# Optimization experiments

Hardware: AMD Instinct MI355X
Metric: run time of the kernel (lower is better)

The kernel has to match this reference:

```python
import jax, jax.numpy as jnp
import numpy as np

N_NODES = 100000
N_EDGES = 1600000
F_IN = 64
H = 64


def gcn_conv(x, W, b, src, dst, ew):
    """PyG GCNConv with edge weights, symmetric norm, self-loops (weight 1)."""
    n = x.shape[0]
    xw = x @ W                                        # [N, H] linear transform first
    deg = jnp.zeros((n,), x.dtype).at[dst].add(ew) + 1.0  # +1 for self-loop weight
    dinv = jax.lax.rsqrt(deg)                         # deg >= 1, safe
    norm = dinv[src] * ew * dinv[dst]                 # [E]
    agg = jnp.zeros_like(xw).at[dst].add(norm[:, None] * xw[src])  # gather-scale-scatter
    agg = agg + (dinv * dinv)[:, None] * xw           # self-loop term: deg^-1 * xw
    return agg + b


def setup_inputs() -> dict:
    key = jax.random.key(0)
    ks = jax.random.split(key, 10)
    x = jax.random.normal(ks[0], (N_NODES, F_IN), jnp.float32)
    edge_index = jax.random.randint(ks[1], (2, N_EDGES), 0, N_NODES, dtype=jnp.int64)
    # distances in km in [0, 500): exp(-(d/200)^2) gives meaningful weight spread
    edge_attr = jax.random.uniform(ks[2], (N_EDGES,), jnp.float32) * 500.0
    s = 1.0 / np.sqrt(H)
    W1 = jax.random.normal(ks[3], (F_IN, H), jnp.float32) * s
    b1 = jnp.zeros((H,), jnp.float32)
    W2 = jax.random.normal(ks[4], (H, H), jnp.float32) * s
    b2 = jnp.zeros((H,), jnp.float32)
    W3 = jax.random.normal(ks[5], (H, 1), jnp.float32) * s
    b3 = jnp.zeros((1,), jnp.float32)
    return {"x": x, "edge_index": edge_index, "edge_attr": edge_attr,
            "W1": W1, "b1": b1, "W2": W2, "b2": b2, "W3": W3, "b3": b3}


def reference(x, edge_index, edge_attr, W1, b1, W2, b2, W3, b3):
    src, dst = edge_index[0], edge_index[1]
    ew = jnp.exp(-jnp.square(edge_attr / 200.0))      # Gaussian distance kernel
    h = jax.nn.relu(gcn_conv(x, W1, b1, src, dst, ew))
    # dropout p=0.1 is identity at eval time (reference runs in eval mode)
    h = jax.nn.relu(gcn_conv(h, W2, b2, src, dst, ew))
    h = gcn_conv(h, W3, b3, src, dst, ew)
    return h[:, 0]                                    # squeeze(-1) -> [N]
```

## Files before the change

kernel.cpp:

```cpp
#include <hip/hip_runtime.h>
#include <cstdint>

#define N_NODES 100000
#define N_EDGES 1600000
#define NBUCKET 196
#define NPB_SHIFT 9
#define NPB 512
#define P1_CHUNK 4096
#define NB_P1 391
#define NBG 1563
#define BSW_CAP 9216
#define CSR_CAP 12800

typedef int iv4 __attribute__((ext_vector_type(4)));
typedef unsigned short usv8 __attribute__((ext_vector_type(8)));

__device__ __forceinline__ unsigned short f2bf(float x) {
    unsigned u = __float_as_uint(x);
    unsigned r = ((u >> 16) & 1u) + 0x7FFFu;
    return (unsigned short)((u + r) >> 16);
}
__device__ __forceinline__ float bf2f(unsigned short v) {
    return __uint_as_float((unsigned)v << 16);
}


__global__ __launch_bounds__(256) void k_init(int* __restrict__ gcursor) {
    int i = threadIdx.x;
    if (i < NBUCKET) gcursor[i] = i * BSW_CAP;
}

struct P1Shared {
    uint2 stage[P1_CHUNK];
    unsigned char stage_bkt[P1_CHUNK];
    int cnt[256];
    int lbase[256];
    int gbase[256];
};
struct GemmShared { float sX[64][65]; float sW[64][65]; };

__global__ __launch_bounds__(256) void k_p1gemm(const int* __restrict__ dst,
                                                const int* __restrict__ srcarr,
                                                const float* __restrict__ ea,
                                                int* gcursor,
                                                uint2* __restrict__ bsw,
                                                const float* __restrict__ X,
                                                const float* __restrict__ W,
                                                float* __restrict__ Y) {
    __shared__ union { P1Shared p; GemmShared g; } sm;
    int t = threadIdx.x;
    if (blockIdx.x < NB_P1) {
        sm.p.cnt[t] = 0;
        __syncthreads();
        int e0 = blockIdx.x * P1_CHUNK;
        unsigned int dr[16];
#pragma unroll
        for (int i = 0; i < 4; ++i) {
            int idx = e0 + (t + i * 256) * 4;
            if (idx + 3 < N_EDGES) {
                int4 d4 = *reinterpret_cast<const int4*>(&dst[idx]);
                int r0 = atomicAdd(&sm.p.cnt[d4.x >> NPB_SHIFT], 1);
                int r1 = atomicAdd(&sm.p.cnt[d4.y >> NPB_SHIFT], 1);
                int r2 = atomicAdd(&sm.p.cnt[d4.z >> NPB_SHIFT], 1);
                int r3 = atomicAdd(&sm.p.cnt[d4.w >> NPB_SHIFT], 1);
                dr[i * 4 + 0] = ((unsigned)d4.x << 12) | (unsigned)r0;
                dr[i * 4 + 1] = ((unsigned)d4.y << 12) | (unsigned)r1;
                dr[i * 4 + 2] = ((unsigned)d4.z << 12) | (unsigned)r2;
                dr[i * 4 + 3] = ((unsigned)d4.w << 12) | (unsigned)r3;
            } else {
#pragma unroll
                for (int k = 0; k < 4; ++k) dr[i * 4 + k] = 0xFFFFFFFFu;
            }
        }
        __syncthreads();
        int v = sm.p.cnt[t];
        sm.p.lbase[t] = v;
        __syncthreads();
        for (int off = 1; off < 256; off <<= 1) {
            int u = (t >= off) ? sm.p.lbase[t - off] : 0;
            __syncthreads();
            sm.p.lbase[t] += u;
            __syncthreads();
        }
        int ex = sm.p.lbase[t] - v;
        if (t < NBUCKET) sm.p.gbase[t] = atomicAdd(&gcursor[t], v);
        __syncthreads();
        sm.p.lbase[t] = ex;
        __syncthreads();
#pragma unroll
        for (int i = 0; i < 4; ++i) {
            int idx = e0 + (t + i * 256) * 4;
            if (idx + 3 < N_EDGES) {
                int4 s4 = *reinterpret_cast<const int4*>(&srcarr[idx]);
                float4 a4 = *reinterpret_cast<const float4*>(&ea[idx]);
                float t0 = a4.x * (1.0f / 200.0f), t1 = a4.y * (1.0f / 200.0f);
                float t2 = a4.z * (1.0f / 200.0f), t3 = a4.w * (1.0f / 200.0f);
                int   ss[4] = {s4.x, s4.y, s4.z, s4.w};
                float ww[4] = {__expf(-t0 * t0), __expf(-t1 * t1),
                               __expf(-t2 * t2), __expf(-t3 * t3)};
#pragma unroll
                for (int k = 0; k < 4; ++k) {
                    unsigned drv = dr[i * 4 + k];
                    int d = drv >> 12, r = drv & 0xFFF;
                    int b = d >> NPB_SHIFT, dloc = d & (NPB - 1);
                    int pos = sm.p.lbase[b] + r;
                    sm.p.stage[pos] = make_uint2(((unsigned)dloc << 17) | (unsigned)ss[k],
                                                 __float_as_uint(ww[k]));
                    sm.p.stage_bkt[pos] = (unsigned char)b;
                }
            }
        }
        __syncthreads();
        int n_valid = min(P1_CHUNK, N_EDGES - e0);
        for (int j = t; j < n_valid; j += 256) {
            int b = sm.p.stage_bkt[j];
            int pos = sm.p.gbase[b] + (j - sm.p.lbase[b]);
            bsw[pos] = sm.p.stage[j];
        }
        return;
    }
    int rb = (blockIdx.x - NB_P1) * 64;
#pragma unroll
    for (int i = 0; i < 16; ++i) {
        int idx = t + i * 256;
        int r = idx >> 6, c = idx & 63;
        sm.g.sW[r][c] = W[idx];
        int gr = rb + r;
        sm.g.sX[r][c] = (gr < N_NODES) ? X[(size_t)gr * 64 + c] : 0.0f;
    }
    __syncthreads();
    int tr = (t >> 4) * 4;
    int tc = (t & 15) * 4;
    float acc[4][4] = {{0.f}};
#pragma unroll 8
    for (int k = 0; k < 64; ++k) {
        float xv[4], wv[4];
#pragma unroll
        for (int i = 0; i < 4; ++i) xv[i] = sm.g.sX[tr + i][k];
#pragma unroll
        for (int j = 0; j < 4; ++j) wv[j] = sm.g.sW[k][tc + j];
#pragma unroll
        for (int i = 0; i < 4; ++i)
#pragma unroll
            for (int j = 0; j < 4; ++j) acc[i][j] = fmaf(xv[i], wv[j], acc[i][j]);
    }
#pragma unroll
    for (int i = 0; i < 4; ++i) {
        int gr = rb + tr + i;
        if (gr < N_NODES) {
            float4 v = make_float4(acc[i][0], acc[i][1], acc[i][2], acc[i][3]);
            *reinterpret_cast<float4*>(&Y[(size_t)gr * 64 + tc]) = v;
        }
    }
}

__global__ __launch_bounds__(1024) void k_p2(const uint2* __restrict__ bsw,
                                             const int* __restrict__ gcursor,
                                             int2* __restrict__ rowinfo,
                                             int2* __restrict__ csr,
                                             float* __restrict__ dinv) {
    __shared__ int cnt[NPB];
    __shared__ int prp[NPB];
    __shared__ int cur[NPB];
    __shared__ float degw[NPB];
    int t = threadIdx.x;
    int b = blockIdx.x;
    if (t < NPB) { cnt[t] = 0; degw[t] = 0.0f; }
    __syncthreads();
    int segb = b * BSW_CAP;
    int sege = gcursor[b];
    int pbase = b * CSR_CAP;
    for (int j = segb + t; j < sege; j += 1024)
        atomicAdd(&cnt[bsw[j].x >> 17], 1);
    __syncthreads();
    int raw = (t < NPB) ? cnt[t] : 0;
    int pad = (raw + 7) & ~7;
    if (t < NPB) prp[t] = pad;
    __syncthreads();
    for (int off = 1; off < NPB; off <<= 1) {
        int u = (t >= off && t < NPB) ? prp[t - off] : 0;
        __syncthreads();
        if (t < NPB) prp[t] += u;
        __syncthreads();
    }
    if (t < NPB) { prp[t] -= pad; cur[t] = prp[t]; }
    __syncthreads();
    int node = (b << NPB_SHIFT) + t;
    if (t < NPB && node < N_NODES)
        rowinfo[node] = make_int2(pbase + prp[t], pad >> 3);
    for (int j = segb + t; j < sege; j += 1024) {
        uint2 v = bsw[j];
        int dloc = (int)(v.x >> 17);
        int src  = (int)(v.x & 0x1FFFFu);
        int pos = atomicAdd(&cur[dloc], 1);
        csr[pbase + pos] = make_int2(src, (int)v.y);
        atomicAdd(&degw[dloc], __uint_as_float(v.y));
    }
    __syncthreads();
    if (t < NPB && node < N_NODES) {
        dinv[node] = rsqrtf(1.0f + degw[t]);
        int begin = pbase + prp[t];
        for (int j = raw; j < pad; ++j) csr[begin + j] = make_int2(node, 0);
    }
}

__global__ __launch_bounds__(256) void k_scale(const float* __restrict__ XW,
                                               const float* __restrict__ dinv,
                                               unsigned short* __restrict__ XWs) {
    int g = blockIdx.x * 256 + threadIdx.x;
    int base = g * 8;
    if (base >= N_NODES * 64) return;
    float d = dinv[base >> 6];
    float4 v0 = *reinterpret_cast<const float4*>(XW + base);
    float4 v1 = *reinterpret_cast<const float4*>(XW + base + 4);
    usv8 r;
    r.s0 = f2bf(d * v0.x); r.s1 = f2bf(d * v0.y);
    r.s2 = f2bf(d * v0.z); r.s3 = f2bf(d * v0.w);
    r.s4 = f2bf(d * v1.x); r.s5 = f2bf(d * v1.y);
    r.s6 = f2bf(d * v1.z); r.s7 = f2bf(d * v1.w);
    *reinterpret_cast<usv8*>(XWs + base) = r;
}


__global__ __launch_bounds__(256) void k_gemm64s(const float* __restrict__ X,
                                                 const float* __restrict__ W,
                                                 const float* __restrict__ dinv,
                                                 unsigned short* __restrict__ XWs) {
    __shared__ float sX[64][65];
    __shared__ float sW[64][65];
    int t = threadIdx.x;
    int rb = blockIdx.x * 64;
#pragma unroll
    for (int i = 0; i < 16; ++i) {
        int idx = t + i * 256;
        int r = idx >> 6, c = idx & 63;
        sW[r][c] = W[idx];
        int gr = rb + r;
        sX[r][c] = (gr < N_NODES) ? X[(size_t)gr * 64 + c] : 0.0f;
    }
    __syncthreads();
    int tr = (t >> 4) * 4;
    int tc = (t & 15) * 4;
    float acc[4][4] = {{0.f}};
#pragma unroll 8
    for (int k = 0; k < 64; ++k) {
        float xv[4], wv[4];
#pragma unroll
        for (int i = 0; i < 4; ++i) xv[i] = sX[tr + i][k];
#pragma unroll
        for (int j = 0; j < 4; ++j) wv[j] = sW[k][tc + j];
#pragma unroll
        for (int i = 0; i < 4; ++i)
#pragma unroll
            for (int j = 0; j < 4; ++j) acc[i][j] = fmaf(xv[i], wv[j], acc[i][j]);
    }
#pragma unroll
    for (int i = 0; i < 4; ++i) {
        int gr = rb + tr + i;
        if (gr < N_NODES) {
            float d = dinv[gr];
            ushort4 v;
            v.x = f2bf(d * acc[i][0]); v.y = f2bf(d * acc[i][1]);
            v.z = f2bf(d * acc[i][2]); v.w = f2bf(d * acc[i][3]);
            *reinterpret_cast<ushort4*>(&XWs[((unsigned)gr << 6) + tc]) = v;
        }
    }
}

template <int MODE>
__global__ __launch_bounds__(256) void k_agg64(const unsigned short* __restrict__ XWs,
                                               const int* __restrict__ csr_i,
                                               const int2* __restrict__ rowinfo,
                                               const float* __restrict__ dinv,
                                               const float* __restrict__ bias,
                                               float* __restrict__ OUT,
                                               const float* __restrict__ W3) {
    int wid0 = (blockIdx.x * 256 + threadIdx.x) >> 6;
    if (wid0 >= N_NODES) return;
    int wid = __builtin_amdgcn_readfirstlane(wid0);
    unsigned f = threadIdx.x & 63;
    float di = dinv[wid];
    float selfs = bf2f(XWs[((unsigned)wid << 6) + f]);
    int2 ri = rowinfo[wid];
    int rbase = __builtin_amdgcn_readfirstlane(ri.x);
    int nb    = __builtin_amdgcn_readfirstlane(ri.y);
    const int* pc = csr_i + ((size_t)rbase * 2);
    float a[8] = {0.f, 0.f, 0.f, 0.f, 0.f, 0.f, 0.f, 0.f};
    for (int it = 0; it < nb; ++it, pc += 16) {
        int s0 = pc[0],  w0 = pc[1],  s1 = pc[2],  w1 = pc[3];
        int s2 = pc[4],  w2 = pc[5],  s3 = pc[6],  w3 = pc[7];
        int s4 = pc[8],  w4 = pc[9],  s5 = pc[10], w5 = pc[11];
        int s6 = pc[12], w6 = pc[13], s7 = pc[14], w7 = pc[15];
        float r0 = bf2f(XWs[((unsigned)s0 << 6) + f]);
        float r1 = bf2f(XWs[((unsigned)s1 << 6) + f]);
        float r2 = bf2f(XWs[((unsigned)s2 << 6) + f]);
        float r3 = bf2f(XWs[((unsigned)s3 << 6) + f]);
        float r4 = bf2f(XWs[((unsigned)s4 << 6) + f]);
        float r5 = bf2f(XWs[((unsigned)s5 << 6) + f]);
        float r6 = bf2f(XWs[((unsigned)s6 << 6) + f]);
        float r7 = bf2f(XWs[((unsigned)s7 << 6) + f]);
        a[0] = fmaf(__int_as_float(w0), r0, a[0]);
        a[1] = fmaf(__int_as_float(w1), r1, a[1]);
        a[2] = fmaf(__int_as_float(w2), r2, a[2]);
        a[3] = fmaf(__int_as_float(w3), r3, a[3]);
        a[4] = fmaf(__int_as_float(w4), r4, a[4]);
        a[5] = fmaf(__int_as_float(w5), r5, a[5]);
        a[6] = fmaf(__int_as_float(w6), r6, a[6]);
        a[7] = fmaf(__int_as_float(w7), r7, a[7]);
    }
    float esum = ((a[0] + a[1]) + (a[2] + a[3])) + ((a[4] + a[5]) + (a[6] + a[7]));
    float acc = di * (selfs + esum) + bias[f];
    acc = fmaxf(acc, 0.0f);
    if (MODE == 0) {
        OUT[((unsigned)wid << 6) + f] = acc;
    } else {
        float v = acc * W3[f];
#pragma unroll
        for (int off = 32; off > 0; off >>= 1) v += __shfl_down(v, off, 64);
        if (f == 0) OUT[wid] = di * v;
    }
}

__global__ __launch_bounds__(256) void k_agg_scalar(const float* __restrict__ xw3s,
                                                    const int2* __restrict__ csr,
                                                    const int2* __restrict__ rowinfo,
                                                    const float* __restrict__ dinv,
                                                    const float* __restrict__ b3,
                                                    float* __restrict__ out) {
    int i = blockIdx.x * 256 + threadIdx.x;
    if (i >= N_NODES) return;
    float di = dinv[i];
    int2 ri = rowinfo[i];
    const iv4* p = reinterpret_cast<const iv4*>(csr + ri.x);
    int nb = ri.y;
    float a0 = 0.f, a1 = 0.f, a2 = 0.f, a3 = 0.f;
    for (int it = 0; it < nb; ++it, p += 4) {
        iv4 q0 = __builtin_nontemporal_load(p);
        iv4 q1 = __builtin_nontemporal_load(p + 1);
        iv4 q2 = __builtin_nontemporal_load(p + 2);
        iv4 q3 = __builtin_nontemporal_load(p + 3);
        a0 = fmaf(__int_as_float(q0.y), xw3s[q0.x], a0);
        a1 = fmaf(__int_as_float(q0.w), xw3s[q0.z], a1);
        a2 = fmaf(__int_as_float(q1.y), xw3s[q1.x], a2);
        a3 = fmaf(__int_as_float(q1.w), xw3s[q1.z], a3);
        a0 = fmaf(__int_as_float(q2.y), xw3s[q2.x], a0);
        a1 = fmaf(__int_as_float(q2.w), xw3s[q2.z], a1);
        a2 = fmaf(__int_as_float(q3.y), xw3s[q3.x], a2);
        a3 = fmaf(__int_as_float(q3.w), xw3s[q3.z], a3);
    }
    out[i] = di * (xw3s[i] + (a0 + a1) + (a2 + a3)) + b3[0];
}


extern "C" void kernel_launch(void* const* d_in, const int* in_sizes, int n_in,
                              void* d_out, int out_size, void* d_ws, size_t ws_size,
                              hipStream_t stream) {
    const float* x  = (const float*)d_in[0];
    const int*   ei = (const int*)d_in[1];
    const float* ea = (const float*)d_in[2];
    const float* W1 = (const float*)d_in[3];
    const float* b1 = (const float*)d_in[4];
    const float* W2 = (const float*)d_in[5];
    const float* b2 = (const float*)d_in[6];
    const float* W3 = (const float*)d_in[7];
    const float* b3 = (const float*)d_in[8];
    float* out = (float*)d_out;
    const int* srcarr = ei;
    const int* dstarr = ei + N_EDGES;

    char* ws = (char*)d_ws;
    size_t off = 0;
    auto alloc = [&](size_t bytes) -> void* {
        void* p = ws + off;
        off = (off + bytes + 255) & ~(size_t)255;
        return p;
    };
    float* dinv     = (float*)alloc((size_t)N_NODES * 4);
    int2*  rowinfo  = (int2*) alloc((size_t)N_NODES * 8);
    int*   gcursor  = (int*)  alloc(NBUCKET * 4);
    float* xw3s     = (float*)alloc((size_t)N_NODES * 4);
    void*  region   = alloc((size_t)NBUCKET * BSW_CAP * 8);
    uint2*          bsw  = (uint2*)region;
    unsigned short* XWs1 = (unsigned short*)region;
    int2*  csr      = (int2*) alloc((size_t)NBUCKET * CSR_CAP * 8);
    float* bufA     = (float*)alloc((size_t)N_NODES * 64 * 4);
    float* bufB     = (float*)alloc((size_t)N_NODES * 64 * 4);
    unsigned short* XWs2 = (unsigned short*)bufA;

    const int nbW = N_NODES / 4;
    const int nbN = (N_NODES + 255) / 256;
    const int nbS = (N_NODES * 64 / 8 + 255) / 256;

    k_init<<<1, 256, 0, stream>>>(gcursor);
    k_p1gemm<<<NB_P1 + NBG, 256, 0, stream>>>(dstarr, srcarr, ea, gcursor,
                                              bsw, x, W1, bufA);
    k_p2<<<NBUCKET, 1024, 0, stream>>>(bsw, gcursor, rowinfo, csr, dinv);
    k_scale<<<nbS, 256, 0, stream>>>(bufA, dinv, XWs1);

    k_agg64<0><<<nbW, 256, 0, stream>>>(XWs1, (const int*)csr, rowinfo, dinv, b1, bufB, nullptr);
    k_gemm64s<<<NBG, 256, 0, stream>>>(bufB, W2, dinv, XWs2);
    k_agg64<1><<<nbW, 256, 0, stream>>>(XWs2, (const int*)csr, rowinfo, dinv, b2, xw3s, W3);
    k_agg_scalar<<<nbN, 256, 0, stream>>>(xw3s, csr, rowinfo, dinv, b3, out);
}
```

Measured before the change: 206.8 us.

## Split wavefront into two half-waves over edges, pad CSR to 16, shrink partition chunks

```diff
diff --git a/kernel.cpp b/kernel.cpp
--- a/kernel.cpp
+++ b/kernel.cpp
@@ -6,11 +6,11 @@
 #define NBUCKET 196
 #define NPB_SHIFT 9
 #define NPB 512
-#define P1_CHUNK 4096
-#define NB_P1 391
+#define P1_CHUNK 2048
+#define NB_P1 782
 #define NBG 1563
 #define BSW_CAP 9216
-#define CSR_CAP 12800
+#define CSR_CAP 17408
 
 typedef int iv4 __attribute__((ext_vector_type(4)));
 typedef unsigned short usv8 __attribute__((ext_vector_type(8)));
@@ -37,7 +37,7 @@
     int lbase[256];
     int gbase[256];
 };
-struct GemmShared { float sX[64][65]; float sW[64][65]; };
+struct GemmShared { float sW[64][65]; float sX[32][65]; };
 
 __global__ __launch_bounds__(256) void k_p1gemm(const int* __restrict__ dst,
                                                 const int* __restrict__ srcarr,
@@ -53,9 +53,9 @@
         sm.p.cnt[t] = 0;
         __syncthreads();
         int e0 = blockIdx.x * P1_CHUNK;
-        unsigned int dr[16];
-#pragma unroll
-        for (int i = 0; i < 4; ++i) {
+        unsigned int dr[8];
+#pragma unroll
+        for (int i = 0; i < 2; ++i) {
             int idx = e0 + (t + i * 256) * 4;
             if (idx + 3 < N_EDGES) {
                 int4 d4 = *reinterpret_cast<const int4*>(&dst[idx]);
@@ -88,7 +88,7 @@
         sm.p.lbase[t] = ex;
         __syncthreads();
 #pragma unroll
-        for (int i = 0; i < 4; ++i) {
+        for (int i = 0; i < 2; ++i) {
             int idx = e0 + (t + i * 256) * 4;
             if (idx + 3 < N_EDGES) {
                 int4 s4 = *reinterpret_cast<const int4*>(&srcarr[idx]);
@@ -123,33 +123,41 @@
 #pragma unroll
     for (int i = 0; i < 16; ++i) {
         int idx = t + i * 256;
-        int r = idx >> 6, c = idx & 63;
-        sm.g.sW[r][c] = W[idx];
-        int gr = rb + r;
-        sm.g.sX[r][c] = (gr < N_NODES) ? X[(size_t)gr * 64 + c] : 0.0f;
-    }
-    __syncthreads();
-    int tr = (t >> 4) * 4;
-    int tc = (t & 15) * 4;
-    float acc[4][4] = {{0.f}};
+        sm.g.sW[idx >> 6][idx & 63] = W[idx];
+    }
+    for (int half = 0; half < 2; ++half) {
+        int rb2 = rb + half * 32;
+        __syncthreads();
+#pragma unroll
+        for (int i = 0; i < 8; ++i) {
+            int idx = t + i * 256;
+            int r = idx >> 6, c = idx & 63;
+            int gr = rb2 + r;
+            sm.g.sX[r][c] = (gr < N_NODES) ? X[(size_t)gr * 64 + c] : 0.0f;
+        }
+        __syncthreads();
+        int tr = (t >> 4) * 2;
+        int tc = (t & 15) * 4;
+        float acc[2][4] = {{0.f, 0.f, 0.f, 0.f}, {0.f, 0.f, 0.f, 0.f}};
 #pragma unroll 8
-    for (int k = 0; k < 64; ++k) {
-        float xv[4], wv[4];
-#pragma unroll
-        for (int i = 0; i < 4; ++i) xv[i] = sm.g.sX[tr + i][k];
-#pragma unroll
-        for (int j = 0; j < 4; ++j) wv[j] = sm.g.sW[k][tc + j];
-#pragma unroll
-        for (int i = 0; i < 4; ++i)
-#pragma unroll
-            for (int j = 0; j < 4; ++j) acc[i][j] = fmaf(xv[i], wv[j], acc[i][j]);
-    }
-#pragma unroll
-    for (int i = 0; i < 4; ++i) {
-        int gr = rb + tr + i;
-        if (gr < N_NODES) {
-            float4 v = make_float4(acc[i][0], acc[i][1], acc[i][2], acc[i][3]);
-            *reinterpret_cast<float4*>(&Y[(size_t)gr * 64 + tc]) = v;
+        for (int k = 0; k < 64; ++k) {
+            float xv0 = sm.g.sX[tr][k], xv1 = sm.g.sX[tr + 1][k];
+            float wv[4];
+#pragma unroll
+            for (int j = 0; j < 4; ++j) wv[j] = sm.g.sW[k][tc + j];
+#pragma unroll
+            for (int j = 0; j < 4; ++j) {
+                acc[0][j] = fmaf(xv0, wv[j], acc[0][j]);
+                acc[1][j] = fmaf(xv1, wv[j], acc[1][j]);
+            }
+        }
+#pragma unroll
+        for (int i = 0; i < 2; ++i) {
+            int gr = rb2 + tr + i;
+            if (gr < N_NODES) {
+                float4 v = make_float4(acc[i][0], acc[i][1], acc[i][2], acc[i][3]);
+                *reinterpret_cast<float4*>(&Y[(size_t)gr * 64 + tc]) = v;
+            }
         }
     }
 }
@@ -174,7 +182,7 @@
         atomicAdd(&cnt[bsw[j].x >> 17], 1);
     __syncthreads();
     int raw = (t < NPB) ? cnt[t] : 0;
-    int pad = (raw + 7) & ~7;
+    int pad = (raw + 15) & ~15;
     if (t < NPB) prp[t] = pad;
     __syncthreads();
     for (int off = 1; off < NPB; off <<= 1) {
@@ -187,7 +195,7 @@
     __syncthreads();
     int node = (b << NPB_SHIFT) + t;
     if (t < NPB && node < N_NODES)
-        rowinfo[node] = make_int2(pbase + prp[t], pad >> 3);
+        rowinfo[node] = make_int2(pbase + prp[t], pad >> 4);
     for (int j = segb + t; j < sege; j += 1024) {
         uint2 v = bsw[j];
         int dloc = (int)(v.x >> 17);
@@ -278,46 +286,71 @@
     int wid0 = (blockIdx.x * 256 + threadIdx.x) >> 6;
     if (wid0 >= N_NODES) return;
     int wid = __builtin_amdgcn_readfirstlane(wid0);
-    unsigned f = threadIdx.x & 63;
+    unsigned lane = threadIdx.x & 63;
+    unsigned q = lane & 31;
+    unsigned h = lane >> 5;
     float di = dinv[wid];
-    float selfs = bf2f(XWs[((unsigned)wid << 6) + f]);
+    unsigned sv = *reinterpret_cast<const unsigned*>(&XWs[((unsigned)wid << 6) + 2u * q]);
     int2 ri = rowinfo[wid];
     int rbase = __builtin_amdgcn_readfirstlane(ri.x);
     int nb    = __builtin_amdgcn_readfirstlane(ri.y);
     const int* pc = csr_i + ((size_t)rbase * 2);
-    float a[8] = {0.f, 0.f, 0.f, 0.f, 0.f, 0.f, 0.f, 0.f};
-    for (int it = 0; it < nb; ++it, pc += 16) {
-        int s0 = pc[0],  w0 = pc[1],  s1 = pc[2],  w1 = pc[3];
-        int s2 = pc[4],  w2 = pc[5],  s3 = pc[6],  w3 = pc[7];
-        int s4 = pc[8],  w4 = pc[9],  s5 = pc[10], w5 = pc[11];
-        int s6 = pc[12], w6 = pc[13], s7 = pc[14], w7 = pc[15];
-        float r0 = bf2f(XWs[((unsigned)s0 << 6) + f]);
-        float r1 = bf2f(XWs[((unsigned)s1 << 6) + f]);
-        float r2 = bf2f(XWs[((unsigned)s2 << 6) + f]);
-        float r3 = bf2f(XWs[((unsigned)s3 << 6) + f]);
-        float r4 = bf2f(XWs[((unsigned)s4 << 6) + f]);
-        float r5 = bf2f(XWs[((unsigned)s5 << 6) + f]);
-        float r6 = bf2f(XWs[((unsigned)s6 << 6) + f]);
-        float r7 = bf2f(XWs[((unsigned)s7 << 6) + f]);
-        a[0] = fmaf(__int_as_float(w0), r0, a[0]);
-        a[1] = fmaf(__int_as_float(w1), r1, a[1]);
-        a[2] = fmaf(__int_as_float(w2), r2, a[2]);
-        a[3] = fmaf(__int_as_float(w3), r3, a[3]);
-        a[4] = fmaf(__int_as_float(w4), r4, a[4]);
-        a[5] = fmaf(__int_as_float(w5), r5, a[5]);
-        a[6] = fmaf(__int_as_float(w6), r6, a[6]);
-        a[7] = fmaf(__int_as_float(w7), r7, a[7]);
-    }
-    float esum = ((a[0] + a[1]) + (a[2] + a[3])) + ((a[4] + a[5]) + (a[6] + a[7]));
-    float acc = di * (selfs + esum) + bias[f];
-    acc = fmaxf(acc, 0.0f);
+    float a0 = 0.f, a1 = 0.f, b0 = 0.f, b1 = 0.f;
+    float c0 = 0.f, c1 = 0.f, d0 = 0.f, d1 = 0.f;
+    for (int it = 0; it < nb; ++it, pc += 32) {
+        int e0 = h ? pc[2]  : pc[0];   float f0 = __int_as_float(h ? pc[3]  : pc[1]);
+        int e1 = h ? pc[6]  : pc[4];   float f1 = __int_as_float(h ? pc[7]  : pc[5]);
+        int e2 = h ? pc[10] : pc[8];   float f2 = __int_as_float(h ? pc[11] : pc[9]);
+        int e3 = h ? pc[14] : pc[12];  float f3 = __int_as_float(h ? pc[15] : pc[13]);
+        int e4 = h ? pc[18] : pc[16];  float f4 = __int_as_float(h ? pc[19] : pc[17]);
+        int e5 = h ? pc[22] : pc[20];  float f5 = __int_as_float(h ? pc[23] : pc[21]);
+        int e6 = h ? pc[26] : pc[24];  float f6 = __int_as_float(h ? pc[27] : pc[25]);
+        int e7 = h ? pc[30] : pc[28];  float f7 = __int_as_float(h ? pc[31] : pc[29]);
+        unsigned v0 = *reinterpret_cast<const unsigned*>(&XWs[((unsigned)e0 << 6) + 2u * q]);
+        unsigned v1 = *reinterpret_cast<const unsigned*>(&XWs[((unsigned)e1 << 6) + 2u * q]);
+        unsigned v2 = *reinterpret_cast<const unsigned*>(&XWs[((unsigned)e2 << 6) + 2u * q]);
+        unsigned v3 = *reinterpret_cast<const unsigned*>(&XWs[((unsigned)e3 << 6) + 2u * q]);
+        unsigned v4 = *reinterpret_cast<const unsigned*>(&XWs[((unsigned)e4 << 6) + 2u * q]);
+        unsigned v5 = *reinterpret_cast<const unsigned*>(&XWs[((unsigned)e5 << 6) + 2u * q]);
+        unsigned v6 = *reinterpret_cast<const unsigned*>(&XWs[((unsigned)e6 << 6) + 2u * q]);
+        unsigned v7 = *reinterpret_cast<const unsigned*>(&XWs[((unsigned)e7 << 6) + 2u * q]);
+        a0 = fmaf(f0, __uint_as_float(v0 << 16), a0);
+        a1 = fmaf(f0, __uint_as_float(v0 & 0xFFFF0000u), a1);
+        b0 = fmaf(f1, __uint_as_float(v1 << 16), b0);
+        b1 = fmaf(f1, __uint_as_float(v1 & 0xFFFF0000u), b1);
+        c0 = fmaf(f2, __uint_as_float(v2 << 16), c0);
+        c1 = fmaf(f2, __uint_as_float(v2 & 0xFFFF0000u), c1);
+        d0 = fmaf(f3, __uint_as_float(v3 << 16), d0);
+        d1 = fmaf(f3, __uint_as_float(v3 & 0xFFFF0000u), d1);
+        a0 = fmaf(f4, __uint_as_float(v4 << 16), a0);
+        a1 = fmaf(f4, __uint_as_float(v4 & 0xFFFF0000u), a1);
+        b0 = fmaf(f5, __uint_as_float(v5 << 16), b0);
+        b1 = fmaf(f5, __uint_as_float(v5 & 0xFFFF0000u), b1);
+        c0 = fmaf(f6, __uint_as_float(v6 << 16), c0);
+        c1 = fmaf(f6, __uint_as_float(v6 & 0xFFFF0000u), c1);
+        d0 = fmaf(f7, __uint_as_float(v7 << 16), d0);
+        d1 = fmaf(f7, __uint_as_float(v7 & 0xFFFF0000u), d1);
+    }
+    float e0sum = (a0 + b0) + (c0 + d0);
+    float e1sum = (a1 + b1) + (c1 + d1);
+    e0sum += __shfl_xor(e0sum, 32, 64);
+    e1sum += __shfl_xor(e1sum, 32, 64);
+    float2 bi = *reinterpret_cast<const float2*>(&bias[2u * q]);
+    float acc0 = di * (__uint_as_float(sv << 16) + e0sum) + bi.x;
+    float acc1 = di * (__uint_as_float(sv & 0xFFFF0000u) + e1sum) + bi.y;
+    acc0 = fmaxf(acc0, 0.0f);
+    acc1 = fmaxf(acc1, 0.0f);
     if (MODE == 0) {
-        OUT[((unsigned)wid << 6) + f] = acc;
+        if (h == 0) {
+            *reinterpret_cast<float2*>(&OUT[((unsigned)wid << 6) + 2u * q]) =
+                make_float2(acc0, acc1);
+        }
     } else {
-        float v = acc * W3[f];
+        float2 w3 = *reinterpret_cast<const float2*>(&W3[2u * q]);
+        float v = acc0 * w3.x + acc1 * w3.y;
 #pragma unroll
         for (int off = 32; off > 0; off >>= 1) v += __shfl_down(v, off, 64);
-        if (f == 0) OUT[wid] = di * v;
+        if (lane == 0) OUT[wid] = di * v * 0.5f;
     }
 }
 
@@ -334,19 +367,22 @@
     const iv4* p = reinterpret_cast<const iv4*>(csr + ri.x);
     int nb = ri.y;
     float a0 = 0.f, a1 = 0.f, a2 = 0.f, a3 = 0.f;
-    for (int it = 0; it < nb; ++it, p += 4) {
-        iv4 q0 = __builtin_nontemporal_load(p);
-        iv4 q1 = __builtin_nontemporal_load(p + 1);
-        iv4 q2 = __builtin_nontemporal_load(p + 2);
-        iv4 q3 = __builtin_nontemporal_load(p + 3);
-        a0 = fmaf(__int_as_float(q0.y), xw3s[q0.x], a0);
-        a1 = fmaf(__int_as_float(q0.w), xw3s[q0.z], a1);
-        a2 = fmaf(__int_as_float(q1.y), xw3s[q1.x], a2);
-        a3 = fmaf(__int_as_float(q1.w), xw3s[q1.z], a3);
-        a0 = fmaf(__int_as_float(q2.y), xw3s[q2.x], a0);
-        a1 = fmaf(__int_as_float(q2.w), xw3s[q2.z], a1);
-        a2 = fmaf(__int_as_float(q3.y), xw3s[q3.x], a2);
-        a3 = fmaf(__int_as_float(q3.w), xw3s[q3.z], a3);
+    for (int it = 0; it < nb; ++it, p += 8) {
+#pragma unroll
+        for (int u = 0; u < 2; ++u) {
+            iv4 q0 = __builtin_nontemporal_load(p + 4 * u);
+            iv4 q1 = __builtin_nontemporal_load(p + 4 * u + 1);
+            iv4 q2 = __builtin_nontemporal_load(p + 4 * u + 2);
+            iv4 q3 = __builtin_nontemporal_load(p + 4 * u + 3);
+            a0 = fmaf(__int_as_float(q0.y), xw3s[q0.x], a0);
+            a1 = fmaf(__int_as_float(q0.w), xw3s[q0.z], a1);
+            a2 = fmaf(__int_as_float(q1.y), xw3s[q1.x], a2);
+            a3 = fmaf(__int_as_float(q1.w), xw3s[q1.z], a3);
+            a0 = fmaf(__int_as_float(q2.y), xw3s[q2.x], a0);
+            a1 = fmaf(__int_as_float(q2.w), xw3s[q2.z], a1);
+            a2 = fmaf(__int_as_float(q3.y), xw3s[q3.x], a2);
+            a3 = fmaf(__int_as_float(q3.w), xw3s[q3.z], a3);
+        }
     }
     out[i] = di * (xw3s[i] + (a0 + a1) + (a2 + a3)) + b3[0];
 }
```

New measurement: 256.2 us. 23.9% more time.

## Shrink bucketing shared memory, use wave-shuffle scan, halve fused GEMM tile rows

Applied to the files above, without the earlier changes.

```diff
diff --git a/kernel.cpp b/kernel.cpp
--- a/kernel.cpp
+++ b/kernel.cpp
@@ -8,7 +8,7 @@
 #define NPB 512
 #define P1_CHUNK 4096
 #define NB_P1 391
-#define NBG 1563
+#define NBG32 3125
 #define BSW_CAP 9216
 #define CSR_CAP 12800
 
@@ -31,13 +31,13 @@
 }
 
 struct P1Shared {
-    uint2 stage[P1_CHUNK];
-    unsigned char stage_bkt[P1_CHUNK];
+    unsigned stage[P1_CHUNK];
     int cnt[256];
     int lbase[256];
     int gbase[256];
+    int wtot[4];
 };
-struct GemmShared { float sX[64][65]; float sW[64][65]; };
+struct GemmShared { float sW[64][65]; float sX[32][65]; };
 
 __global__ __launch_bounds__(256) void k_p1gemm(const int* __restrict__ dst,
                                                 const int* __restrict__ srcarr,
@@ -74,78 +74,81 @@
         }
         __syncthreads();
         int v = sm.p.cnt[t];
-        sm.p.lbase[t] = v;
-        __syncthreads();
-        for (int off = 1; off < 256; off <<= 1) {
-            int u = (t >= off) ? sm.p.lbase[t - off] : 0;
-            __syncthreads();
-            sm.p.lbase[t] += u;
-            __syncthreads();
-        }
-        int ex = sm.p.lbase[t] - v;
+        int lane = t & 63, wv = t >> 6;
+        int x = v;
+#pragma unroll
+        for (int off = 1; off < 64; off <<= 1) {
+            int y = __shfl_up(x, off, 64);
+            if (lane >= off) x += y;
+        }
+        if (lane == 63) sm.p.wtot[wv] = x;
         if (t < NBUCKET) sm.p.gbase[t] = atomicAdd(&gcursor[t], v);
         __syncthreads();
-        sm.p.lbase[t] = ex;
+        int pre = 0;
+#pragma unroll
+        for (int w = 0; w < 4; ++w) pre += (w < wv) ? sm.p.wtot[w] : 0;
+        sm.p.lbase[t] = pre + x - v;
         __syncthreads();
 #pragma unroll
         for (int i = 0; i < 4; ++i) {
-            int idx = e0 + (t + i * 256) * 4;
-            if (idx + 3 < N_EDGES) {
-                int4 s4 = *reinterpret_cast<const int4*>(&srcarr[idx]);
-                float4 a4 = *reinterpret_cast<const float4*>(&ea[idx]);
-                float t0 = a4.x * (1.0f / 200.0f), t1 = a4.y * (1.0f / 200.0f);
-                float t2 = a4.z * (1.0f / 200.0f), t3 = a4.w * (1.0f / 200.0f);
-                int   ss[4] = {s4.x, s4.y, s4.z, s4.w};
-                float ww[4] = {__expf(-t0 * t0), __expf(-t1 * t1),
-                               __expf(-t2 * t2), __expf(-t3 * t3)};
-#pragma unroll
-                for (int k = 0; k < 4; ++k) {
-                    unsigned drv = dr[i * 4 + k];
+#pragma unroll
+            for (int k = 0; k < 4; ++k) {
+                unsigned drv = dr[i * 4 + k];
+                if (drv != 0xFFFFFFFFu) {
                     int d = drv >> 12, r = drv & 0xFFF;
-                    int b = d >> NPB_SHIFT, dloc = d & (NPB - 1);
-                    int pos = sm.p.lbase[b] + r;
-                    sm.p.stage[pos] = make_uint2(((unsigned)dloc << 17) | (unsigned)ss[k],
-                                                 __float_as_uint(ww[k]));
-                    sm.p.stage_bkt[pos] = (unsigned char)b;
+                    int b = d >> NPB_SHIFT;
+                    int le = (t + i * 256) * 4 + k;
+                    sm.p.stage[sm.p.lbase[b] + r] = ((unsigned)d << 12) | (unsigned)le;
                 }
             }
         }
         __syncthreads();
         int n_valid = min(P1_CHUNK, N_EDGES - e0);
         for (int j = t; j < n_valid; j += 256) {
-            int b = sm.p.stage_bkt[j];
+            unsigned sv = sm.p.stage[j];
+            int d = sv >> 12, le = sv & 0xFFF;
+            int b = d >> NPB_SHIFT, dloc = d & (NPB - 1);
+            int s = srcarr[e0 + le];
+            float aa = ea[e0 + le];
+            float tt = aa * (1.0f / 200.0f);
+            float w = __expf(-tt * tt);
             int pos = sm.p.gbase[b] + (j - sm.p.lbase[b]);
-            bsw[pos] = sm.p.stage[j];
+            bsw[pos] = make_uint2(((unsigned)dloc << 17) | (unsigned)s,
+                                  __float_as_uint(w));
         }
         return;
     }
-    int rb = (blockIdx.x - NB_P1) * 64;
+    int rb = (blockIdx.x - NB_P1) * 32;
 #pragma unroll
     for (int i = 0; i < 16; ++i) {
         int idx = t + i * 256;
+        sm.g.sW[idx >> 6][idx & 63] = W[idx];
+    }
+#pragma unroll
+    for (int i = 0; i < 8; ++i) {
+        int idx = t + i * 256;
         int r = idx >> 6, c = idx & 63;
-        sm.g.sW[r][c] = W[idx];
         int gr = rb + r;
         sm.g.sX[r][c] = (gr < N_NODES) ? X[(size_t)gr * 64 + c] : 0.0f;
     }
     __syncthreads();
-    int tr = (t >> 4) * 4;
+    int tr = (t >> 4) * 2;
     int tc = (t & 15) * 4;
-    float acc[4][4] = {{0.f}};
+    float acc[2][4] = {{0.f, 0.f, 0.f, 0.f}, {0.f, 0.f, 0.f, 0.f}};
 #pragma unroll 8
     for (int k = 0; k < 64; ++k) {
-        float xv[4], wv[4];
-#pragma unroll
-        for (int i = 0; i < 4; ++i) xv[i] = sm.g.sX[tr + i][k];
+        float xv0 = sm.g.sX[tr][k], xv1 = sm.g.sX[tr + 1][k];
+        float wv[4];
 #pragma unroll
         for (int j = 0; j < 4; ++j) wv[j] = sm.g.sW[k][tc + j];
 #pragma unroll
-        for (int i = 0; i < 4; ++i)
-#pragma unroll
-            for (int j = 0; j < 4; ++j) acc[i][j] = fmaf(xv[i], wv[j], acc[i][j]);
-    }
-#pragma unroll
-    for (int i = 0; i < 4; ++i) {
+        for (int j = 0; j < 4; ++j) {
+            acc[0][j] = fmaf(xv0, wv[j], acc[0][j]);
+            acc[1][j] = fmaf(xv1, wv[j], acc[1][j]);
+        }
+    }
+#pragma unroll
+    for (int i = 0; i < 2; ++i) {
         int gr = rb + tr + i;
         if (gr < N_NODES) {
             float4 v = make_float4(acc[i][0], acc[i][1], acc[i][2], acc[i][3]);
@@ -392,13 +395,13 @@
     const int nbS = (N_NODES * 64 / 8 + 255) / 256;
 
     k_init<<<1, 256, 0, stream>>>(gcursor);
-    k_p1gemm<<<NB_P1 + NBG, 256, 0, stream>>>(dstarr, srcarr, ea, gcursor,
-                                              bsw, x, W1, bufA);
+    k_p1gemm<<<NB_P1 + NBG32, 256, 0, stream>>>(dstarr, srcarr, ea, gcursor,
+                                                bsw, x, W1, bufA);
     k_p2<<<NBUCKET, 1024, 0, stream>>>(bsw, gcursor, rowinfo, csr, dinv);
     k_scale<<<nbS, 256, 0, stream>>>(bufA, dinv, XWs1);
 
     k_agg64<0><<<nbW, 256, 0, stream>>>(XWs1, (const int*)csr, rowinfo, dinv, b1, bufB, nullptr);
-    k_gemm64s<<<NBG, 256, 0, stream>>>(bufB, W2, dinv, XWs2);
+    k_gemm64s<<<(N_NODES + 63) / 64, 256, 0, stream>>>(bufB, W2, dinv, XWs2);
     k_agg64<1><<<nbW, 256, 0, stream>>>(XWs2, (const int*)csr, rowinfo, dinv, b2, xw3s, W3);
     k_agg_scalar<<<nbN, 256, 0, stream>>>(xw3s, csr, rowinfo, dinv, b3, out);
 }
```

Measured after the change: 210.3 us. About the same (+1.7%).
